# Kernel tuning notes

Measured on AMD Instinct MI355X. Metric: run time of the kernel, lower is better.

Reference implementation:

```python
import jax, jax.numpy as jnp
import numpy as np

N_NODES = 50000
N_EDGES = 800000
IN_DIM = 512
HID_DIM = 128


def setup_inputs() -> dict:
    key = jax.random.key(0)
    k1, k2, k3 = jax.random.split(key, 3)
    x = jax.random.normal(k1, (N_NODES, IN_DIM), dtype=jnp.float32)
    edge_index = jax.random.randint(k2, (2, N_EDGES), 0, N_NODES, dtype=jnp.int32)
    # GCNConv weight (glorot-ish scale) and bias
    W = jax.random.normal(k3, (IN_DIM, HID_DIM), dtype=jnp.float32) * (1.0 / np.sqrt(IN_DIM))
    b = jnp.zeros((HID_DIM,), dtype=jnp.float32)
    # PReLU per-channel slope, torch default init 0.25
    prelu_w = jnp.full((HID_DIM,), 0.25, dtype=jnp.float32)
    return {"x": x, "edge_index": edge_index, "W": W, "b": b, "prelu_w": prelu_w}


def reference(x, edge_index, W, b, prelu_w):
    N = x.shape[0]
    # 1) linear transform first (GCNConv transforms then aggregates)
    h = x @ W  # [N, H]
    # 2) add self-loops
    loop = jnp.arange(N, dtype=edge_index.dtype)
    src = jnp.concatenate([edge_index[0], loop])  # [E+N]
    dst = jnp.concatenate([edge_index[1], loop])  # [E+N]
    # 3) symmetric degree normalization deg^-1/2 (self-loops guarantee deg>=1)
    deg = jax.ops.segment_sum(jnp.ones_like(dst, dtype=h.dtype), dst, num_segments=N)
    dinv = jax.lax.rsqrt(deg)
    norm = dinv[src] * dinv[dst]  # [E+N]
    # 4) gather-scale-scatter aggregation
    msg = h[src] * norm[:, None]  # [E+N, H]
    out = jax.ops.segment_sum(msg, dst, num_segments=N) + b  # [N, H]
    # 5) per-channel PReLU
    return jnp.where(out > 0, out, prelu_w * out)
```

## Files before the change

kernel.cpp:

```cpp
#include <hip/hip_runtime.h>

#define IN_DIM 512
#define HID 128
#define BK 64

#define RANGE 98
#define NB_ 511
#define NBLK 200
#define SEGCAP 2048

typedef float f4 __attribute__((ext_vector_type(4)));
typedef short bf8 __attribute__((ext_vector_type(8)));

__device__ inline unsigned short f2bf(float f) {
    unsigned u = __float_as_uint(f);
    unsigned r = (u + 0x7FFFu + ((u >> 16) & 1u)) >> 16;
    return (unsigned short)r;
}
__device__ inline float bf2f(unsigned short u) {
    return __uint_as_float(((unsigned)u) << 16);
}
__device__ inline int xcd_perm(int blk) {
    return (blk & 7) * (NBLK / 8) + (blk >> 3);
}

__global__ __launch_bounds__(256) void k_count(const int* __restrict__ dst,
                                               int* __restrict__ cmat, int E) {
    __shared__ int bins[NB_];
    const int blk = blockIdx.x, t = threadIdx.x;
    const int chunk = (((E + NBLK - 1) / NBLK) + 3) & ~3;
    const int start = blk * chunk;
    const int end = min(E, start + chunk);
    for (int i = t; i < NB_; i += 256) bins[i] = 0;
    __syncthreads();
    if (start < E) {
        int nvec = (end - start) >> 2;
        for (int i = t; i < nvec; i += 256) {
            int4 d4 = *(const int4*)(dst + start + i * 4);
            atomicAdd(&bins[d4.x / RANGE], 1);
            atomicAdd(&bins[d4.y / RANGE], 1);
            atomicAdd(&bins[d4.z / RANGE], 1);
            atomicAdd(&bins[d4.w / RANGE], 1);
        }
        for (int i = start + nvec * 4 + t; i < end; i += 256)
            atomicAdd(&bins[dst[i] / RANGE], 1);
    }
    __syncthreads();
    const int p = xcd_perm(blk);
    for (int j = t; j < NB_; j += 256) cmat[j * NBLK + p] = bins[j];
}

__global__ __launch_bounds__(256) void k_cscan(int* __restrict__ cmat,
                                               int* __restrict__ tot) {
    __shared__ int s[256];
    const int j = blockIdx.x, t = threadIdx.x;
    int v = (t < NBLK) ? cmat[j * NBLK + t] : 0;
    s[t] = v;
    __syncthreads();
    for (int off = 1; off < 256; off <<= 1) {
        int y = (t >= off) ? s[t - off] : 0;
        __syncthreads();
        s[t] += y;
        __syncthreads();
    }
    if (t < NBLK) cmat[j * NBLK + t] = s[t] - v;
    if (t == 255) tot[j] = s[255];
}

__global__ __launch_bounds__(512) void k_tscan(const int* __restrict__ tot,
                                               int* __restrict__ bbase,
                                               int* __restrict__ rowStart,
                                               int N, int E) {
    __shared__ int s[512];
    int t = threadIdx.x;
    int v = (t < NB_) ? tot[t] : 0;
    s[t] = v;
    __syncthreads();
    for (int off = 1; off < 512; off <<= 1) {
        int y = (t >= off) ? s[t - off] : 0;
        __syncthreads();
        s[t] += y;
        __syncthreads();
    }
    if (t < NB_) bbase[t] = s[t] - v;
    if (t == 0) rowStart[N] = E;
}

__global__ __launch_bounds__(256) void k_scatter(const int* __restrict__ src,
                                                 const int* __restrict__ dst,
                                                 const int* __restrict__ cmat,
                                                 const int* __restrict__ bbase,
                                                 unsigned* __restrict__ ebuf, int E) {
    __shared__ int cur[NB_];
    const int blk = blockIdx.x, t = threadIdx.x;
    const int p = xcd_perm(blk);
    for (int j = t; j < NB_; j += 256) cur[j] = bbase[j] + cmat[j * NBLK + p];
    __syncthreads();
    const int chunk = (((E + NBLK - 1) / NBLK) + 3) & ~3;
    const int start = blk * chunk;
    const int end = min(E, start + chunk);
    if (start >= E) return;
    int nvec = (end - start) >> 2;
    for (int i = t; i < nvec; i += 256) {
        int4 s4 = *(const int4*)(src + start + i * 4);
        int4 d4 = *(const int4*)(dst + start + i * 4);
        int ss[4] = {s4.x, s4.y, s4.z, s4.w};
        int dd[4] = {d4.x, d4.y, d4.z, d4.w};
#pragma unroll
        for (int k = 0; k < 4; k++) {
            int b = dd[k] / RANGE;
            int ld = dd[k] - b * RANGE;
            int pos = atomicAdd(&cur[b], 1);
            ebuf[pos] = ((unsigned)ld << 25) | (unsigned)ss[k];
        }
    }
    for (int i = start + nvec * 4 + t; i < end; i += 256) {
        int d = dst[i];
        int b = d / RANGE;
        int ld = d - b * RANGE;
        int pos = atomicAdd(&cur[b], 1);
        ebuf[pos] = ((unsigned)ld << 25) | (unsigned)src[i];
    }
}

__global__ __launch_bounds__(256) void k_binfill(const unsigned* __restrict__ ebuf,
                                                 const int* __restrict__ tot,
                                                 const int* __restrict__ bbase,
                                                 int* __restrict__ rowStart,
                                                 float* __restrict__ dinv,
                                                 int* __restrict__ esrc, int N) {
    __shared__ int bins[RANGE];
    __shared__ int cur[RANGE];
    __shared__ int ss[128];
    __shared__ int seg[SEGCAP];
    const int b = blockIdx.x;
    const int t = threadIdx.x;
    const int base = bbase[b];
    const int cnt = min(tot[b], SEGCAP);
    const int n0 = b * RANGE;
    const unsigned* ep = ebuf + base;

    for (int i = t; i < RANGE; i += 256) bins[i] = 0;
    __syncthreads();
    for (int i = t; i < cnt; i += 256) atomicAdd(&bins[ep[i] >> 25], 1);
    __syncthreads();
    int v = (t < RANGE) ? bins[t] : 0;
    if (t < 128) ss[t] = v;
    __syncthreads();
    for (int off = 1; off < 128; off <<= 1) {
        int y = (t >= off && t < 128) ? ss[t - off] : 0;
        __syncthreads();
        if (t < 128) ss[t] += y;
        __syncthreads();
    }
    if (t < RANGE) {
        int ex = ss[t] - v;
        cur[t] = ex;
        int g = n0 + t;
        if (g < N) {
            rowStart[g] = base + ex;
            dinv[g] = rsqrtf((float)(v + 1));
        }
    }
    __syncthreads();
    for (int i = t; i < cnt; i += 256) {
        unsigned w = ep[i];
        int r = atomicAdd(&cur[w >> 25], 1);
        if (r < SEGCAP) seg[r] = (int)(w & 0x1FFFFFFu);
    }
    __syncthreads();
    for (int i = t; i < cnt; i += 256) esrc[base + i] = seg[i];
}

__global__ __launch_bounds__(256) void k_convW(const float* __restrict__ W,
                                               unsigned short* __restrict__ Wt) {
    int id = blockIdx.x * 256 + threadIdx.x;
    int n = id & (HID - 1);
    int k = id >> 7;
    Wt[(size_t)n * IN_DIM + k] = f2bf(W[(size_t)k * HID + n]);
}

__global__ __launch_bounds__(256, 2) void k_gemm(const float* __restrict__ x,
                                                 const unsigned short* __restrict__ Wt,
                                                 unsigned short* __restrict__ h, int M) {
    __shared__ unsigned short As[128][BK + 8];
    __shared__ unsigned short Bs[128][BK + 8];
    const int t = threadIdx.x;
    const int wave = t >> 6, lane = t & 63;
    const int row0 = blockIdx.x * 128;
    const int quad = lane >> 4, l16 = lane & 15;

    f4 acc[2][8];
#pragma unroll
    for (int i = 0; i < 2; i++)
#pragma unroll
        for (int j = 0; j < 8; j++) acc[i][j] = (f4){0.f, 0.f, 0.f, 0.f};

    const int srow = t >> 1;
    const int shalf = t & 1;
    const bool rowok = (row0 + srow) < M;
    const float* xrow = x + (size_t)(row0 + srow) * IN_DIM + shalf * 32;
    const unsigned short* wrow = Wt + (size_t)srow * IN_DIM + shalf * 32;

    for (int k0 = 0; k0 < IN_DIM; k0 += BK) {
        float4 v[8];
#pragma unroll
        for (int i = 0; i < 8; i++)
            v[i] = rowok ? *(const float4*)(xrow + k0 + i * 4)
                         : make_float4(0.f, 0.f, 0.f, 0.f);
        unsigned short tmp[32];
#pragma unroll
        for (int i = 0; i < 8; i++) {
            tmp[i * 4 + 0] = f2bf(v[i].x);
            tmp[i * 4 + 1] = f2bf(v[i].y);
            tmp[i * 4 + 2] = f2bf(v[i].z);
            tmp[i * 4 + 3] = f2bf(v[i].w);
        }
#pragma unroll
        for (int i = 0; i < 4; i++)
            *(float4*)&As[srow][shalf * 32 + i * 8] = *(float4*)&tmp[i * 8];
#pragma unroll
        for (int i = 0; i < 4; i++)
            *(float4*)&Bs[srow][shalf * 32 + i * 8] =
                *(const float4*)(wrow + k0 + i * 8);
        __syncthreads();

#pragma unroll
        for (int ks = 0; ks < BK; ks += 32) {
            bf8 af[2];
#pragma unroll
            for (int rt = 0; rt < 2; rt++)
                af[rt] = *(const bf8*)&As[wave * 32 + rt * 16 + l16][ks + quad * 8];
#pragma unroll
            for (int nt = 0; nt < 8; nt++) {
                bf8 bfv = *(const bf8*)&Bs[nt * 16 + l16][ks + quad * 8];
#pragma unroll
                for (int rt = 0; rt < 2; rt++)
                    acc[rt][nt] = __builtin_amdgcn_mfma_f32_16x16x32_bf16(
                        af[rt], bfv, acc[rt][nt], 0, 0, 0);
            }
        }
        __syncthreads();
    }

#pragma unroll
    for (int rt = 0; rt < 2; rt++) {
#pragma unroll
        for (int reg = 0; reg < 4; reg++) {
            int row = row0 + wave * 32 + rt * 16 + quad * 4 + reg;
            if (row < M) {
#pragma unroll
                for (int nt = 0; nt < 8; nt++) {
                    int col = nt * 16 + l16;
                    h[(size_t)row * HID + col] = f2bf(acc[rt][nt][reg]);
                }
            }
        }
    }
}

__global__ __launch_bounds__(256) void k_pull(const unsigned short* __restrict__ h,
                                              const int* __restrict__ esrc,
                                              const int* __restrict__ rowStart,
                                              const float* __restrict__ dinv,
                                              const float* __restrict__ bias,
                                              const float* __restrict__ pw,
                                              float* __restrict__ out, int N) {
    int gid = blockIdx.x * 256 + threadIdx.x;
    int node = gid >> 5;
    int l = threadIdx.x & 31;
    if (node >= N) return;
    int e0 = rowStart[node], e1 = rowStart[node + 1];
    float di = dinv[node];
    const int ci = l * 4;
    ushort4 hv = *(const ushort4*)&h[(size_t)node * HID + ci];
    float s2 = di * di;
    float ax = bf2f(hv.x) * s2, ay = bf2f(hv.y) * s2;
    float az = bf2f(hv.z) * s2, aw = bf2f(hv.w) * s2;
    int j = e0;
    for (; j + 4 <= e1; j += 4) {
        int s0 = esrc[j], s1 = esrc[j + 1], s2i = esrc[j + 2], s3 = esrc[j + 3];
        float w0 = dinv[s0] * di, w1 = dinv[s1] * di;
        float w2 = dinv[s2i] * di, w3 = dinv[s3] * di;
        ushort4 a0 = *(const ushort4*)&h[(size_t)s0 * HID + ci];
        ushort4 a1 = *(const ushort4*)&h[(size_t)s1 * HID + ci];
        ushort4 a2 = *(const ushort4*)&h[(size_t)s2i * HID + ci];
        ushort4 a3 = *(const ushort4*)&h[(size_t)s3 * HID + ci];
        ax += bf2f(a0.x) * w0 + bf2f(a1.x) * w1 + bf2f(a2.x) * w2 + bf2f(a3.x) * w3;
        ay += bf2f(a0.y) * w0 + bf2f(a1.y) * w1 + bf2f(a2.y) * w2 + bf2f(a3.y) * w3;
        az += bf2f(a0.z) * w0 + bf2f(a1.z) * w1 + bf2f(a2.z) * w2 + bf2f(a3.z) * w3;
        aw += bf2f(a0.w) * w0 + bf2f(a1.w) * w1 + bf2f(a2.w) * w2 + bf2f(a3.w) * w3;
    }
    for (; j < e1; j++) {
        int s = esrc[j];
        float w = dinv[s] * di;
        ushort4 a = *(const ushort4*)&h[(size_t)s * HID + ci];
        ax += bf2f(a.x) * w; ay += bf2f(a.y) * w;
        az += bf2f(a.z) * w; aw += bf2f(a.w) * w;
    }
    float4 bv = *(const float4*)&bias[ci];
    float4 pv = *(const float4*)&pw[ci];
    float ox = ax + bv.x, oy = ay + bv.y, oz = az + bv.z, ow = aw + bv.w;
    ox = ox > 0.f ? ox : pv.x * ox;
    oy = oy > 0.f ? oy : pv.y * oy;
    oz = oz > 0.f ? oz : pv.z * oz;
    ow = ow > 0.f ? ow : pv.w * ow;
    *(float4*)&out[(size_t)node * HID + ci] = make_float4(ox, oy, oz, ow);
}

extern "C" void kernel_launch(void* const* d_in, const int* in_sizes, int n_in,
                              void* d_out, int out_size, void* d_ws, size_t ws_size,
                              hipStream_t stream) {
    const float* x  = (const float*)d_in[0];
    const int*   ei = (const int*)d_in[1];
    const float* W  = (const float*)d_in[2];
    const float* b  = (const float*)d_in[3];
    const float* pw = (const float*)d_in[4];

    const int N = in_sizes[0] / IN_DIM;
    const int E = in_sizes[1] / 2;
    const int* src = ei;
    const int* dst = ei + E;

    char* ws = (char*)d_ws;
    size_t off = 0;
    auto carve = [&](size_t bytes) -> void* {
        void* p = ws + off;
        off = (off + bytes + 255) & ~(size_t)255;
        return p;
    };
    unsigned short* h = (unsigned short*)carve((size_t)N * HID * sizeof(unsigned short));
    int*   rowStart = (int*)carve((size_t)(N + 1) * sizeof(int));
    float* dinv     = (float*)carve((size_t)N * sizeof(float));
    int*   esrc     = (int*)carve((size_t)E * sizeof(int));
    unsigned short* Wt = (unsigned short*)carve((size_t)IN_DIM * HID * sizeof(unsigned short));
    int*   cmat     = (int*)carve((size_t)NB_ * NBLK * sizeof(int));
    int*   tot      = (int*)carve((size_t)NB_ * sizeof(int));
    int*   bbase    = (int*)carve((size_t)NB_ * sizeof(int));
    unsigned* ebuf  = (unsigned*)carve((size_t)E * sizeof(unsigned));

    k_convW<<<(IN_DIM * HID) / 256, 256, 0, stream>>>(W, Wt);
    k_gemm<<<(N + 127) / 128, 256, 0, stream>>>(x, Wt, h, N);
    k_count<<<NBLK, 256, 0, stream>>>(dst, cmat, E);
    k_cscan<<<NB_, 256, 0, stream>>>(cmat, tot);
    k_tscan<<<1, 512, 0, stream>>>(tot, bbase, rowStart, N, E);
    k_scatter<<<NBLK, 256, 0, stream>>>(src, dst, cmat, bbase, ebuf, E);
    k_binfill<<<NB_, 256, 0, stream>>>(ebuf, tot, bbase, rowStart, dinv, esrc, N);
    k_pull<<<(int)(((size_t)N * 32 + 255) / 256), 256, 0, stream>>>(
        h, esrc, rowStart, dinv, b, pw, (float*)d_out, N);
}
```

Measured before the change: 236.9 us.

## Prescale GEMM output by dinv and widen pull to 8 channels per lane

The GEMM epilogue now multiplies each row of h by dinv[row], so the pull kernel no longer gathers dinv for each source edge and instead scales the summed neighbours once by the destination's dinv. To make that possible the GEMM launch moves after the degree/CSR build. The pull kernel also uses 16 lanes per node with 8-channel bf16 loads instead of 32 lanes with 4 channels, halving the threads per node and issuing wider gather loads. Rounding changes slightly because the normalisation is applied before the bf16 conversion, and the GEMM can no longer overlap with the graph preprocessing stages.

Result: no change. 235.9 us (-0.4%).

```diff
diff --git a/kernel.cpp b/kernel.cpp
--- a/kernel.cpp
+++ b/kernel.cpp
@@ -182,6 +182,7 @@
 
 __global__ __launch_bounds__(256, 2) void k_gemm(const float* __restrict__ x,
                                                  const unsigned short* __restrict__ Wt,
+                                                 const float* __restrict__ dinv,
                                                  unsigned short* __restrict__ h, int M) {
     __shared__ unsigned short As[128][BK + 8];
     __shared__ unsigned short Bs[128][BK + 8];
@@ -249,10 +250,11 @@
         for (int reg = 0; reg < 4; reg++) {
             int row = row0 + wave * 32 + rt * 16 + quad * 4 + reg;
             if (row < M) {
+                float dv = dinv[row];
 #pragma unroll
                 for (int nt = 0; nt < 8; nt++) {
                     int col = nt * 16 + l16;
-                    h[(size_t)row * HID + col] = f2bf(acc[rt][nt][reg]);
+                    h[(size_t)row * HID + col] = f2bf(acc[rt][nt][reg] * dv);
                 }
             }
         }
@@ -267,45 +269,48 @@
                                               const float* __restrict__ pw,
                                               float* __restrict__ out, int N) {
     int gid = blockIdx.x * 256 + threadIdx.x;
-    int node = gid >> 5;
-    int l = threadIdx.x & 31;
+    int node = gid >> 4;
+    int l = threadIdx.x & 15;
     if (node >= N) return;
     int e0 = rowStart[node], e1 = rowStart[node + 1];
     float di = dinv[node];
-    const int ci = l * 4;
-    ushort4 hv = *(const ushort4*)&h[(size_t)node * HID + ci];
-    float s2 = di * di;
-    float ax = bf2f(hv.x) * s2, ay = bf2f(hv.y) * s2;
-    float az = bf2f(hv.z) * s2, aw = bf2f(hv.w) * s2;
+    const int ci = l * 8;
+    bf8 hv = *(const bf8*)&h[(size_t)node * HID + ci];
+    float a[8];
+#pragma unroll
+    for (int c = 0; c < 8; c++) a[c] = bf2f((unsigned short)hv[c]);
     int j = e0;
     for (; j + 4 <= e1; j += 4) {
-        int s0 = esrc[j], s1 = esrc[j + 1], s2i = esrc[j + 2], s3 = esrc[j + 3];
-        float w0 = dinv[s0] * di, w1 = dinv[s1] * di;
-        float w2 = dinv[s2i] * di, w3 = dinv[s3] * di;
-        ushort4 a0 = *(const ushort4*)&h[(size_t)s0 * HID + ci];
-        ushort4 a1 = *(const ushort4*)&h[(size_t)s1 * HID + ci];
-        ushort4 a2 = *(const ushort4*)&h[(size_t)s2i * HID + ci];
-        ushort4 a3 = *(const ushort4*)&h[(size_t)s3 * HID + ci];
-        ax += bf2f(a0.x) * w0 + bf2f(a1.x) * w1 + bf2f(a2.x) * w2 + bf2f(a3.x) * w3;
-        ay += bf2f(a0.y) * w0 + bf2f(a1.y) * w1 + bf2f(a2.y) * w2 + bf2f(a3.y) * w3;
-        az += bf2f(a0.z) * w0 + bf2f(a1.z) * w1 + bf2f(a2.z) * w2 + bf2f(a3.z) * w3;
-        aw += bf2f(a0.w) * w0 + bf2f(a1.w) * w1 + bf2f(a2.w) * w2 + bf2f(a3.w) * w3;
+        int s0 = esrc[j], s1 = esrc[j + 1], s2 = esrc[j + 2], s3 = esrc[j + 3];
+        bf8 r0 = *(const bf8*)&h[(size_t)s0 * HID + ci];
+        bf8 r1 = *(const bf8*)&h[(size_t)s1 * HID + ci];
+        bf8 r2 = *(const bf8*)&h[(size_t)s2 * HID + ci];
+        bf8 r3 = *(const bf8*)&h[(size_t)s3 * HID + ci];
+#pragma unroll
+        for (int c = 0; c < 8; c++)
+            a[c] += bf2f((unsigned short)r0[c]) + bf2f((unsigned short)r1[c]) +
+                    bf2f((unsigned short)r2[c]) + bf2f((unsigned short)r3[c]);
     }
     for (; j < e1; j++) {
         int s = esrc[j];
-        float w = dinv[s] * di;
-        ushort4 a = *(const ushort4*)&h[(size_t)s * HID + ci];
-        ax += bf2f(a.x) * w; ay += bf2f(a.y) * w;
-        az += bf2f(a.z) * w; aw += bf2f(a.w) * w;
-    }
-    float4 bv = *(const float4*)&bias[ci];
-    float4 pv = *(const float4*)&pw[ci];
-    float ox = ax + bv.x, oy = ay + bv.y, oz = az + bv.z, ow = aw + bv.w;
-    ox = ox > 0.f ? ox : pv.x * ox;
-    oy = oy > 0.f ? oy : pv.y * oy;
-    oz = oz > 0.f ? oz : pv.z * oz;
-    ow = ow > 0.f ? ow : pv.w * ow;
-    *(float4*)&out[(size_t)node * HID + ci] = make_float4(ox, oy, oz, ow);
+        bf8 r = *(const bf8*)&h[(size_t)s * HID + ci];
+#pragma unroll
+        for (int c = 0; c < 8; c++) a[c] += bf2f((unsigned short)r[c]);
+    }
+    float4 b0 = *(const float4*)&bias[ci];
+    float4 b1 = *(const float4*)&bias[ci + 4];
+    float4 p0 = *(const float4*)&pw[ci];
+    float4 p1 = *(const float4*)&pw[ci + 4];
+    float ob[8] = {b0.x, b0.y, b0.z, b0.w, b1.x, b1.y, b1.z, b1.w};
+    float op[8] = {p0.x, p0.y, p0.z, p0.w, p1.x, p1.y, p1.z, p1.w};
+    float o[8];
+#pragma unroll
+    for (int c = 0; c < 8; c++) {
+        float v = a[c] * di + ob[c];
+        o[c] = v > 0.f ? v : op[c] * v;
+    }
+    *(float4*)&out[(size_t)node * HID + ci]     = make_float4(o[0], o[1], o[2], o[3]);
+    *(float4*)&out[(size_t)node * HID + ci + 4] = make_float4(o[4], o[5], o[6], o[7]);
 }
 
 extern "C" void kernel_launch(void* const* d_in, const int* in_sizes, int n_in,
@@ -340,12 +345,12 @@
     unsigned* ebuf  = (unsigned*)carve((size_t)E * sizeof(unsigned));
 
     k_convW<<<(IN_DIM * HID) / 256, 256, 0, stream>>>(W, Wt);
-    k_gemm<<<(N + 127) / 128, 256, 0, stream>>>(x, Wt, h, N);
     k_count<<<NBLK, 256, 0, stream>>>(dst, cmat, E);
     k_cscan<<<NB_, 256, 0, stream>>>(cmat, tot);
     k_tscan<<<1, 512, 0, stream>>>(tot, bbase, rowStart, N, E);
     k_scatter<<<NBLK, 256, 0, stream>>>(src, dst, cmat, bbase, ebuf, E);
     k_binfill<<<NB_, 256, 0, stream>>>(ebuf, tot, bbase, rowStart, dinv, esrc, N);
-    k_pull<<<(int)(((size_t)N * 32 + 255) / 256), 256, 0, stream>>>(
+    k_gemm<<<(N + 127) / 128, 256, 0, stream>>>(x, Wt, dinv, h, N);
+    k_pull<<<(int)(((size_t)N * 16 + 255) / 256), 256, 0, stream>>>(
         h, esrc, rowStart, dinv, b, pw, (float*)d_out, N);
 }
```
